# Performance work log

Hardware: AMD Instinct MI355X
Metric: run time of the kernel (lower is better)

Reference implementation:

```python
import jax, jax.numpy as jnp
import numpy as np

K = 15                # top-k codes per token
COMMITMENT_COST = 0.25
N, D, Q = 16384, 256, 8192  # tokens, embed_dim, quant_dim (codebook size)


def setup_inputs() -> dict:
    key = jax.random.key(0)
    k1, k2 = jax.random.split(key)
    z_e = jax.random.normal(k1, (N, D), dtype=jnp.float32)
    # codebook initialized uniform(-1/Q, 1/Q) as in the torch module
    embedding = jax.random.uniform(k2, (Q, D), dtype=jnp.float32,
                                   minval=-1.0 / Q, maxval=1.0 / Q)
    return {"z_e": z_e, "embedding": embedding}


def reference(z_e, embedding):
    # squared L2 distances: [N, Q]
    dist = (jnp.sum(z_e ** 2, axis=1, keepdims=True)
            - 2.0 * (z_e @ embedding.T)
            + jnp.sum(embedding ** 2, axis=1)[None, :])
    # top-k nearest codes (torch.topk(-dist))
    _, top_k_indices = jax.lax.top_k(-dist, K)           # [N, K] int32
    z_q_k = embedding[top_k_indices]                      # [N, K, D] gather
    # k-hot scatter: [N, Q]
    rows = jnp.arange(z_e.shape[0])[:, None]              # [N, 1]
    k_hot = jnp.zeros((z_e.shape[0], embedding.shape[0]), dtype=z_e.dtype)
    k_hot = k_hot.at[rows, top_k_indices].set(1.0)
    z_q = jnp.sum(z_q_k, axis=1)                          # [N, D]
    vq_loss = jnp.mean((z_q - jax.lax.stop_gradient(z_e)) ** 2)
    commitment_loss = jnp.mean((z_e - jax.lax.stop_gradient(z_q)) ** 2)
    total_vq_loss = vq_loss + COMMITMENT_COST * commitment_loss
    # straight-through estimator
    z_q_ste = z_e + jax.lax.stop_gradient(z_q - z_e)
    return (z_q_ste, total_vq_loss, k_hot)
```

## Files before the change

### kernel.cpp

```cpp
#include <hip/hip_runtime.h>


#pragma clang fp contract(off)

#define DIM   256
#define KSEL  15
#define CAP   160
#define NTC   64
#define NTO   32
#define KR    24

typedef short  s16x8 __attribute__((ext_vector_type(8)));
typedef float  f32x4 __attribute__((ext_vector_type(4)));

__device__ inline unsigned short f2bf(float f) {
  unsigned u = __builtin_bit_cast(unsigned, f);
  unsigned r = (u + 0x7FFFu + ((u >> 16) & 1u)) >> 16;
  return (unsigned short)r;
}

__device__ inline void nt_zero4(float* p) {
  f32x4 v = {0.f, 0.f, 0.f, 0.f};
  __builtin_nontemporal_store(v, (f32x4*)p);
}

__global__ __launch_bounds__(256)
void prep(const float* __restrict__ emb, unsigned short* __restrict__ ebf,
          float* __restrict__ Enp, int Q) {
  const int gid = blockIdx.x * 256 + threadIdx.x;
  {
    const int i = gid * 8;
    float4 a = *(const float4*)(emb + i);
    float4 b = *(const float4*)(emb + i + 4);
    ushort4 o0; o0.x = f2bf(a.x); o0.y = f2bf(a.y); o0.z = f2bf(a.z); o0.w = f2bf(a.w);
    ushort4 o1; o1.x = f2bf(b.x); o1.y = f2bf(b.y); o1.z = f2bf(b.z); o1.w = f2bf(b.w);
    *(ushort4*)(ebf + i) = o0;
    *(ushort4*)(ebf + i + 4) = o1;
  }
  if (gid < Q) {
    const float* ep = emb + (size_t)gid * DIM;
    float Eh[2];
    for (int h = 0; h < 2; ++h) {
      const int base = 128 * h;
      float r[8];
#pragma unroll
      for (int q2 = 0; q2 < 8; ++q2) { float v = ep[base + q2]; r[q2] = v * v; }
      for (int i = 8; i < 128; i += 8)
#pragma unroll
        for (int q2 = 0; q2 < 8; ++q2) { float v = ep[base + i + q2]; float sq = v * v; r[q2] = r[q2] + sq; }
      Eh[h] = ((r[0] + r[1]) + (r[2] + r[3])) + ((r[4] + r[5]) + (r[6] + r[7]));
    }
    Enp[gid] = Eh[0] + Eh[1];
  }
}

__global__ __launch_bounds__(512, 2)
void vq_capture(const float* __restrict__ z, const unsigned short* __restrict__ ebf,
                int* __restrict__ cntg, unsigned short* __restrict__ candg,
                int N, int Q) {
  __shared__ union {
    unsigned short zbf[NTC][264];
    struct {
      unsigned short candL[NTC][CAP + 2];
      float          scL[NTC][CAP + 1];
    } c;
  } U;
  __shared__ int   cntL[NTC];
  __shared__ float tauL[NTC];
  __shared__ float red[512];

  const int tid  = threadIdx.x;
  const int lane = tid & 63;
  const int wv   = tid >> 6;
  const int t0   = blockIdx.x * NTC;

  {
    const int rt = tid >> 3, rq = tid & 7;
    const float* zp = z + (size_t)(t0 + rt) * DIM;
    float s = 0.f;
#pragma unroll
    for (int m = 0; m < 8; ++m) {
      float4 v = *(const float4*)(zp + 4 * rq + 32 * m);
      s = __builtin_fmaf(v.x, v.x, s);
      s = __builtin_fmaf(v.y, v.y, s);
      s = __builtin_fmaf(v.z, v.z, s);
      s = __builtin_fmaf(v.w, v.w, s);
      ushort4 o; o.x = f2bf(v.x); o.y = f2bf(v.y); o.z = f2bf(v.z); o.w = f2bf(v.w);
      *(ushort4*)&U.zbf[rt][4 * rq + 32 * m] = o;
    }
    red[tid] = s;
  }
  if (tid < NTC) cntL[tid] = 0;
  __syncthreads();

  if (tid < NTC) {
    float s = 0.f;
    for (int j = 0; j < 8; ++j) s += red[tid * 8 + j];
    const float a = 1.0f / (float)Q;
    tauL[tid] = 2.45f * a * 0.57735027f * sqrtf(s) - 1e-6f;
  }

  s16x8 afrag[4][8];
  {
    const int arow = lane & 15;
    const int kq   = (lane >> 4) * 8;
#pragma unroll
    for (int tt = 0; tt < 4; ++tt) {
#pragma unroll
      for (int ks = 0; ks < 8; ++ks)
        afrag[tt][ks] = *(const s16x8*)&U.zbf[tt * 16 + arow][ks * 32 + kq];
    }
  }
  __syncthreads();

  {
    const int ncw  = Q / 8;
    const int c0w  = wv * ncw;
    const int col  = lane & 15;
    const int kq8  = (lane >> 4) * 8;
    const int rbase = (lane >> 4) * 4;
    const unsigned short* bbase = ebf + ((size_t)(c0w + col) * DIM + kq8);

    uint4 buf0[8], buf1[8];
#pragma unroll
    for (int ks = 0; ks < 8; ++ks) buf0[ks] = *(const uint4*)(bbase + ks * 32);

    for (int it = 0; it < 64; it += 2) {
      {
        const unsigned short* bp = bbase + (size_t)(it + 1) * 16 * DIM;
#pragma unroll
        for (int ks = 0; ks < 8; ++ks) buf1[ks] = *(const uint4*)(bp + ks * 32);
      }
      {
        f32x4 acc0 = {0.f, 0.f, 0.f, 0.f};
        f32x4 acc1 = {0.f, 0.f, 0.f, 0.f};
        f32x4 acc2 = {0.f, 0.f, 0.f, 0.f};
        f32x4 acc3 = {0.f, 0.f, 0.f, 0.f};
#pragma unroll
        for (int ks = 0; ks < 8; ++ks) {
          s16x8 bfv = __builtin_bit_cast(s16x8, buf0[ks]);
          acc0 = __builtin_amdgcn_mfma_f32_16x16x32_bf16(afrag[0][ks], bfv, acc0, 0, 0, 0);
          acc1 = __builtin_amdgcn_mfma_f32_16x16x32_bf16(afrag[1][ks], bfv, acc1, 0, 0, 0);
          acc2 = __builtin_amdgcn_mfma_f32_16x16x32_bf16(afrag[2][ks], bfv, acc2, 0, 0, 0);
          acc3 = __builtin_amdgcn_mfma_f32_16x16x32_bf16(afrag[3][ks], bfv, acc3, 0, 0, 0);
        }
        const int code = c0w + it * 16 + col;
#pragma unroll
        for (int r = 0; r < 4; ++r) {
          const int tk0 = rbase + r;
          if (acc0[r] > tauL[tk0]) {
            int s = atomicAdd(&cntL[tk0], 1);
            if (s < CAP) { U.c.candL[tk0][s] = (unsigned short)code; U.c.scL[tk0][s] = acc0[r]; }
          }
          const int tk1 = 16 + rbase + r;
          if (acc1[r] > tauL[tk1]) {
            int s = atomicAdd(&cntL[tk1], 1);
            if (s < CAP) { U.c.candL[tk1][s] = (unsigned short)code; U.c.scL[tk1][s] = acc1[r]; }
          }
          const int tk2 = 32 + rbase + r;
          if (acc2[r] > tauL[tk2]) {
            int s = atomicAdd(&cntL[tk2], 1);
            if (s < CAP) { U.c.candL[tk2][s] = (unsigned short)code; U.c.scL[tk2][s] = acc2[r]; }
          }
          const int tk3 = 48 + rbase + r;
          if (acc3[r] > tauL[tk3]) {
            int s = atomicAdd(&cntL[tk3], 1);
            if (s < CAP) { U.c.candL[tk3][s] = (unsigned short)code; U.c.scL[tk3][s] = acc3[r]; }
          }
        }
      }
      if (it + 2 < 64) {
        const unsigned short* bp = bbase + (size_t)(it + 2) * 16 * DIM;
#pragma unroll
        for (int ks = 0; ks < 8; ++ks) buf0[ks] = *(const uint4*)(bp + ks * 32);
      }
      {
        f32x4 acc0 = {0.f, 0.f, 0.f, 0.f};
        f32x4 acc1 = {0.f, 0.f, 0.f, 0.f};
        f32x4 acc2 = {0.f, 0.f, 0.f, 0.f};
        f32x4 acc3 = {0.f, 0.f, 0.f, 0.f};
#pragma unroll
        for (int ks = 0; ks < 8; ++ks) {
          s16x8 bfv = __builtin_bit_cast(s16x8, buf1[ks]);
          acc0 = __builtin_amdgcn_mfma_f32_16x16x32_bf16(afrag[0][ks], bfv, acc0, 0, 0, 0);
          acc1 = __builtin_amdgcn_mfma_f32_16x16x32_bf16(afrag[1][ks], bfv, acc1, 0, 0, 0);
          acc2 = __builtin_amdgcn_mfma_f32_16x16x32_bf16(afrag[2][ks], bfv, acc2, 0, 0, 0);
          acc3 = __builtin_amdgcn_mfma_f32_16x16x32_bf16(afrag[3][ks], bfv, acc3, 0, 0, 0);
        }
        const int code = c0w + (it + 1) * 16 + col;
#pragma unroll
        for (int r = 0; r < 4; ++r) {
          const int tk0 = rbase + r;
          if (acc0[r] > tauL[tk0]) {
            int s = atomicAdd(&cntL[tk0], 1);
            if (s < CAP) { U.c.candL[tk0][s] = (unsigned short)code; U.c.scL[tk0][s] = acc0[r]; }
          }
          const int tk1 = 16 + rbase + r;
          if (acc1[r] > tauL[tk1]) {
            int s = atomicAdd(&cntL[tk1], 1);
            if (s < CAP) { U.c.candL[tk1][s] = (unsigned short)code; U.c.scL[tk1][s] = acc1[r]; }
          }
          const int tk2 = 32 + rbase + r;
          if (acc2[r] > tauL[tk2]) {
            int s = atomicAdd(&cntL[tk2], 1);
            if (s < CAP) { U.c.candL[tk2][s] = (unsigned short)code; U.c.scL[tk2][s] = acc2[r]; }
          }
          const int tk3 = 48 + rbase + r;
          if (acc3[r] > tauL[tk3]) {
            int s = atomicAdd(&cntL[tk3], 1);
            if (s < CAP) { U.c.candL[tk3][s] = (unsigned short)code; U.c.scL[tk3][s] = acc3[r]; }
          }
        }
      }
    }
  }
  __syncthreads();

  if ((tid & 7) == 0) {
    const int t = tid >> 3;
    const int m = min(cntL[t], CAP);
    const int keep = min(m, KR);
    for (int k = 0; k < keep; ++k) {
      float bv = -3.4e38f; int bj = 0;
      for (int j = 0; j < m; ++j) {
        float v = U.c.scL[t][j];
        if (v > bv) { bv = v; bj = j; }
      }
      U.c.scL[t][bj] = -3.5e38f;
      candg[(size_t)(t0 + t) * KR + k] = U.c.candL[t][bj];
    }
    cntg[t0 + t] = keep;
  }
}

__global__ __launch_bounds__(256, 2)
void vq_out(const float* __restrict__ z, const float* __restrict__ emb,
            const float* __restrict__ Enp, const int* __restrict__ cntg,
            const unsigned short* __restrict__ candg, float* __restrict__ out,
            int N, int Q) {
  __shared__ __align__(16) float zlds[NTO][DIM + 4];
  __shared__ __align__(16) float ebuf[KR][DIM + 4];
  __shared__ unsigned short cand[NTO][KR];
  __shared__ float sc[NTO][KR + 1];
  __shared__ int   cntL[NTO];
  __shared__ float ArowL[NTO];
  __shared__ int   win[NTO][KSEL];
  __shared__ float red[256];

  const int tid = threadIdx.x;
  const int t0  = blockIdx.x * NTO;
  float* khot = out + (size_t)N * DIM + 1;
  float* pref = khot + (size_t)t0 * Q + 3;
  const int nf4 = (NTO * Q - 4) / 4;

  if (tid < 3) khot[(size_t)t0 * Q + tid] = 0.f;
  if (tid == 3) khot[(size_t)t0 * Q + (size_t)NTO * Q - 1] = 0.f;

  {
    const int rt = tid >> 3, rq = tid & 7;
    const float* zp = z + (size_t)(t0 + rt) * DIM;
    float4 tmp[8];
#pragma unroll
    for (int m = 0; m < 8; ++m) tmp[m] = *(const float4*)(zp + 4 * rq + 32 * m);
#pragma unroll
    for (int m = 0; m < 8; ++m) *(float4*)&zlds[rt][4 * rq + 32 * m] = tmp[m];
  }
  if (tid < NTO) cntL[tid] = min(cntg[t0 + tid], KR);
  __syncthreads();

  for (int i = tid; i < NTO * KR; i += 256) {
    const int t = i / KR, s = i - t * KR;
    cand[t][s] = candg[(size_t)(t0 + t) * KR + s];
  }

  if (tid < NTO) {
    const float* zl = &zlds[tid][0];
    float Ah[2];
    for (int h = 0; h < 2; ++h) {
      const int base = 128 * h;
      float r[8];
#pragma unroll
      for (int q2 = 0; q2 < 8; ++q2) { float v = zl[base + q2]; r[q2] = v * v; }
      for (int i = 8; i < 128; i += 8)
#pragma unroll
        for (int q2 = 0; q2 < 8; ++q2) { float v = zl[base + i + q2]; float sq = v * v; r[q2] = r[q2] + sq; }
      Ah[h] = ((r[0] + r[1]) + (r[2] + r[3])) + ((r[4] + r[5]) + (r[6] + r[7]));
    }
    ArowL[tid] = Ah[0] + Ah[1];
  }
  __syncthreads();

  for (int b = 0; b < NTO; ++b) {
    const int mb = cntL[b];
    {
      const int row = tid >> 3, rq = tid & 7;
      if (row < mb) {
        const float* ep = emb + (size_t)cand[b][row] * DIM;
        float4 tmp[8];
#pragma unroll
        for (int m = 0; m < 8; ++m) tmp[m] = *(const float4*)(ep + 4 * rq + 32 * m);
#pragma unroll
        for (int m = 0; m < 8; ++m) *(float4*)&ebuf[row][4 * rq + 32 * m] = tmp[m];
      }
    }
    {
      const int i0 = b * 2048 + tid;
#pragma unroll
      for (int k = 0; k < 8; ++k) {
        const int i = i0 + k * 256;
        if (i < nf4) nt_zero4(pref + 4 * (size_t)i);
      }
    }
    __syncthreads();
    if ((tid & 7) == 0) {
      const int ci = tid >> 3;
      if (ci < mb) {
        const float* el = &ebuf[ci][0];
        const float* zl = &zlds[b][0];
        float bch = 0.f;
        for (int i = 0; i < 256; i += 8) {
          float4 ea = *(const float4*)(el + i);
          float4 eb = *(const float4*)(el + i + 4);
          float4 za = *(const float4*)(zl + i);
          float4 zb = *(const float4*)(zl + i + 4);
          bch = __builtin_fmaf(za.x, ea.x, bch);
          bch = __builtin_fmaf(za.y, ea.y, bch);
          bch = __builtin_fmaf(za.z, ea.z, bch);
          bch = __builtin_fmaf(za.w, ea.w, bch);
          bch = __builtin_fmaf(zb.x, eb.x, bch);
          bch = __builtin_fmaf(zb.y, eb.y, bch);
          bch = __builtin_fmaf(zb.z, eb.z, bch);
          bch = __builtin_fmaf(zb.w, eb.w, bch);
        }
        const int c = cand[b][ci];
        sc[b][ci] = (ArowL[b] - 2.0f * bch) + Enp[c];
      } else if (ci < KR) {
        sc[b][ci] = 3.4e38f;
      }
    }
    __syncthreads();
  }

  if (tid < NTO) {
    const int m = cntL[tid];
    for (int k = 0; k < KSEL; ++k) {
      float bv = 3.4e38f; int bc = 0x7fffffff; int bj = -1;
      for (int j = 0; j < m; ++j) {
        float v = sc[tid][j]; int c = cand[tid][j];
        if (v < bv || (v == bv && c < bc)) { bv = v; bc = c; bj = j; }
      }
      if (bj >= 0) sc[tid][bj] = 3.5e38f;
      win[tid][k] = (bj >= 0) ? bc : 0;
    }
  }
  __syncthreads();

  {
    const int qt = tid >> 3, qq = tid & 7;
    float4 zq4[8];
#pragma unroll
    for (int m = 0; m < 8; ++m) zq4[m] = make_float4(0.f, 0.f, 0.f, 0.f);
    for (int k = 0; k < KSEL; ++k) {
      const int c = win[qt][k];
      const float* ep = emb + (size_t)c * DIM;
#pragma unroll
      for (int m = 0; m < 8; ++m) {
        float4 e4 = *(const float4*)(ep + 4 * qq + 32 * m);
        zq4[m].x = zq4[m].x + e4.x; zq4[m].y = zq4[m].y + e4.y;
        zq4[m].z = zq4[m].z + e4.z; zq4[m].w = zq4[m].w + e4.w;
      }
    }
    float* op = out + (size_t)(t0 + qt) * DIM;
    float lp = 0.f;
#pragma unroll
    for (int m = 0; m < 8; ++m) {
      float4 zv = *(const float4*)&zlds[qt][4 * qq + 32 * m];
      float4 qv = zq4[m];
      float d0 = qv.x - zv.x, d1 = qv.y - zv.y, d2 = qv.z - zv.z, d3 = qv.w - zv.w;
      float4 o; o.x = zv.x + d0; o.y = zv.y + d1; o.z = zv.z + d2; o.w = zv.w + d3;
      *(float4*)(op + 4 * qq + 32 * m) = o;
      lp = __builtin_fmaf(d0, d0, lp);
      lp = __builtin_fmaf(d1, d1, lp);
      lp = __builtin_fmaf(d2, d2, lp);
      lp = __builtin_fmaf(d3, d3, lp);
    }
    red[tid] = lp;
  }
  __syncthreads();
  for (int s = 128; s > 0; s >>= 1) {
    if (tid < s) red[tid] += red[tid + s];
    __syncthreads();
  }
  if (tid == 0) {
    const float scale = 1.25f / (float)((size_t)N * DIM);
    atomicAdd(out + (size_t)N * DIM, red[0] * scale);
  }

  for (int i = tid; i < NTO * KSEL; i += 256) {
    const int t = i / KSEL, k = i - t * KSEL;
    khot[(size_t)(t0 + t) * Q + win[t][k]] = 1.0f;
  }
}

extern "C" void kernel_launch(void* const* d_in, const int* in_sizes, int n_in,
                              void* d_out, int out_size, void* d_ws, size_t ws_size,
                              hipStream_t stream) {
  const float* z   = (const float*)d_in[0];
  const float* emb = (const float*)d_in[1];
  float* out = (float*)d_out;
  const int N = in_sizes[0] / DIM;
  const int Q = in_sizes[1] / DIM;

  unsigned short* ebf = (unsigned short*)d_ws;
  char* p = (char*)d_ws + (size_t)Q * DIM * 2;
  float* Enp  = (float*)p;           p += (size_t)Q * 4;
  int*   cntg = (int*)p;             p += (size_t)N * 4;
  unsigned short* candg = (unsigned short*)p;

  hipMemsetAsync((char*)d_out + (size_t)N * DIM * sizeof(float), 0, sizeof(float), stream);
  prep<<<dim3((Q * DIM) / (8 * 256)), dim3(256), 0, stream>>>(emb, ebf, Enp, Q);
  vq_capture<<<dim3(N / NTC), dim3(512), 0, stream>>>(z, ebf, cntg, candg, N, Q);
  vq_out<<<dim3(N / NTO), dim3(256), 0, stream>>>(z, emb, Enp, cntg, candg, out, N, Q);
}
```

Measured before the change: 896.0 us.

## Restructure vq_out to one wavefront per token with shuffle-based top-k

Rewrites the final rescoring kernel so that each 64-lane wavefront handles four tokens in turn. Each lane scores one candidate straight from global memory, and the top-15 is picked with a 64-bit key min-reduction over wave shuffles. This replaces block-wide LDS staging of candidate rows, per-token __syncthreads, and single-thread serial selection. The k-hot row zeroing moves to ordinary stores per wave, and the ones are written after a vmcnt wait. In exchange, occupancy rises, but each lane's dot product now reads embedding rows uncoalesced from global memory, and the nontemporal stores for the large zero fill are dropped.

```diff
diff --git a/kernel.cpp b/kernel.cpp
--- a/kernel.cpp
+++ b/kernel.cpp
@@ -7,7 +7,6 @@
 #define KSEL  15
 #define CAP   160
 #define NTC   64
-#define NTO   32
 #define KR    24
 
 typedef short  s16x8 __attribute__((ext_vector_type(8)));
@@ -17,11 +16,6 @@
   unsigned u = __builtin_bit_cast(unsigned, f);
   unsigned r = (u + 0x7FFFu + ((u >> 16) & 1u)) >> 16;
   return (unsigned short)r;
-}
-
-__device__ inline void nt_zero4(float* p) {
-  f32x4 v = {0.f, 0.f, 0.f, 0.f};
-  __builtin_nontemporal_store(v, (f32x4*)p);
 }
 
 __global__ __launch_bounds__(256)
@@ -233,159 +227,133 @@
   }
 }
 
-__global__ __launch_bounds__(256, 2)
+__global__ __launch_bounds__(256, 4)
 void vq_out(const float* __restrict__ z, const float* __restrict__ emb,
             const float* __restrict__ Enp, const int* __restrict__ cntg,
             const unsigned short* __restrict__ candg, float* __restrict__ out,
             int N, int Q) {
-  __shared__ __align__(16) float zlds[NTO][DIM + 4];
-  __shared__ __align__(16) float ebuf[KR][DIM + 4];
-  __shared__ unsigned short cand[NTO][KR];
-  __shared__ float sc[NTO][KR + 1];
-  __shared__ int   cntL[NTO];
-  __shared__ float ArowL[NTO];
-  __shared__ int   win[NTO][KSEL];
+  __shared__ __align__(16) float zld[4][DIM + 4];
   __shared__ float red[256];
 
-  const int tid = threadIdx.x;
-  const int t0  = blockIdx.x * NTO;
+  const int tid  = threadIdx.x;
+  const int lane = tid & 63;
+  const int wv   = tid >> 6;
+  const int gw   = blockIdx.x * 4 + wv;
   float* khot = out + (size_t)N * DIM + 1;
-  float* pref = khot + (size_t)t0 * Q + 3;
-  const int nf4 = (NTO * Q - 4) / 4;
-
-  if (tid < 3) khot[(size_t)t0 * Q + tid] = 0.f;
-  if (tid == 3) khot[(size_t)t0 * Q + (size_t)NTO * Q - 1] = 0.f;
-
-  {
-    const int rt = tid >> 3, rq = tid & 7;
-    const float* zp = z + (size_t)(t0 + rt) * DIM;
-    float4 tmp[8];
-#pragma unroll
-    for (int m = 0; m < 8; ++m) tmp[m] = *(const float4*)(zp + 4 * rq + 32 * m);
-#pragma unroll
-    for (int m = 0; m < 8; ++m) *(float4*)&zlds[rt][4 * rq + 32 * m] = tmp[m];
-  }
-  if (tid < NTO) cntL[tid] = min(cntg[t0 + tid], KR);
-  __syncthreads();
-
-  for (int i = tid; i < NTO * KR; i += 256) {
-    const int t = i / KR, s = i - t * KR;
-    cand[t][s] = candg[(size_t)(t0 + t) * KR + s];
-  }
-
-  if (tid < NTO) {
-    const float* zl = &zlds[tid][0];
-    float Ah[2];
-    for (int h = 0; h < 2; ++h) {
-      const int base = 128 * h;
-      float r[8];
-#pragma unroll
-      for (int q2 = 0; q2 < 8; ++q2) { float v = zl[base + q2]; r[q2] = v * v; }
-      for (int i = 8; i < 128; i += 8)
-#pragma unroll
-        for (int q2 = 0; q2 < 8; ++q2) { float v = zl[base + i + q2]; float sq = v * v; r[q2] = r[q2] + sq; }
-      Ah[h] = ((r[0] + r[1]) + (r[2] + r[3])) + ((r[4] + r[5]) + (r[6] + r[7]));
-    }
-    ArowL[tid] = Ah[0] + Ah[1];
-  }
-  __syncthreads();
-
-  for (int b = 0; b < NTO; ++b) {
-    const int mb = cntL[b];
-    {
-      const int row = tid >> 3, rq = tid & 7;
-      if (row < mb) {
-        const float* ep = emb + (size_t)cand[b][row] * DIM;
-        float4 tmp[8];
-#pragma unroll
-        for (int m = 0; m < 8; ++m) tmp[m] = *(const float4*)(ep + 4 * rq + 32 * m);
-#pragma unroll
-        for (int m = 0; m < 8; ++m) *(float4*)&ebuf[row][4 * rq + 32 * m] = tmp[m];
-      }
-    }
-    {
-      const int i0 = b * 2048 + tid;
-#pragma unroll
-      for (int k = 0; k < 8; ++k) {
-        const int i = i0 + k * 256;
-        if (i < nf4) nt_zero4(pref + 4 * (size_t)i);
-      }
-    }
-    __syncthreads();
-    if ((tid & 7) == 0) {
-      const int ci = tid >> 3;
-      if (ci < mb) {
-        const float* el = &ebuf[ci][0];
-        const float* zl = &zlds[b][0];
-        float bch = 0.f;
-        for (int i = 0; i < 256; i += 8) {
-          float4 ea = *(const float4*)(el + i);
-          float4 eb = *(const float4*)(el + i + 4);
-          float4 za = *(const float4*)(zl + i);
-          float4 zb = *(const float4*)(zl + i + 4);
-          bch = __builtin_fmaf(za.x, ea.x, bch);
-          bch = __builtin_fmaf(za.y, ea.y, bch);
-          bch = __builtin_fmaf(za.z, ea.z, bch);
-          bch = __builtin_fmaf(za.w, ea.w, bch);
-          bch = __builtin_fmaf(zb.x, eb.x, bch);
-          bch = __builtin_fmaf(zb.y, eb.y, bch);
-          bch = __builtin_fmaf(zb.z, eb.z, bch);
-          bch = __builtin_fmaf(zb.w, eb.w, bch);
-        }
-        const int c = cand[b][ci];
-        sc[b][ci] = (ArowL[b] - 2.0f * bch) + Enp[c];
-      } else if (ci < KR) {
-        sc[b][ci] = 3.4e38f;
-      }
-    }
-    __syncthreads();
-  }
-
-  if (tid < NTO) {
-    const int m = cntL[tid];
-    for (int k = 0; k < KSEL; ++k) {
-      float bv = 3.4e38f; int bc = 0x7fffffff; int bj = -1;
-      for (int j = 0; j < m; ++j) {
-        float v = sc[tid][j]; int c = cand[tid][j];
-        if (v < bv || (v == bv && c < bc)) { bv = v; bc = c; bj = j; }
-      }
-      if (bj >= 0) sc[tid][bj] = 3.5e38f;
-      win[tid][k] = (bj >= 0) ? bc : 0;
-    }
-  }
-  __syncthreads();
-
-  {
-    const int qt = tid >> 3, qq = tid & 7;
-    float4 zq4[8];
-#pragma unroll
-    for (int m = 0; m < 8; ++m) zq4[m] = make_float4(0.f, 0.f, 0.f, 0.f);
-    for (int k = 0; k < KSEL; ++k) {
-      const int c = win[qt][k];
-      const float* ep = emb + (size_t)c * DIM;
-#pragma unroll
-      for (int m = 0; m < 8; ++m) {
-        float4 e4 = *(const float4*)(ep + 4 * qq + 32 * m);
-        zq4[m].x = zq4[m].x + e4.x; zq4[m].y = zq4[m].y + e4.y;
-        zq4[m].z = zq4[m].z + e4.z; zq4[m].w = zq4[m].w + e4.w;
-      }
-    }
-    float* op = out + (size_t)(t0 + qt) * DIM;
-    float lp = 0.f;
-#pragma unroll
-    for (int m = 0; m < 8; ++m) {
-      float4 zv = *(const float4*)&zlds[qt][4 * qq + 32 * m];
-      float4 qv = zq4[m];
-      float d0 = qv.x - zv.x, d1 = qv.y - zv.y, d2 = qv.z - zv.z, d3 = qv.w - zv.w;
+
+  float lpacc = 0.f;
+
+  for (int ti = 0; ti < 4; ++ti) {
+    const int t = gw * 4 + ti;
+
+    {
+      const float4 v = *(const float4*)(z + (size_t)t * DIM + 4 * lane);
+      *(float4*)&zld[wv][4 * lane] = v;
+    }
+    const int mb = min(cntg[t], KR);
+    const int c_mine = (lane < mb) ? (int)candg[(size_t)t * KR + lane] : 0;
+
+    __builtin_amdgcn_s_waitcnt(0);
+
+    float Arow;
+    {
+      float Aval = 0.f;
+      if (lane == 0) {
+        const float* zl = &zld[wv][0];
+        float Ah[2];
+        for (int h = 0; h < 2; ++h) {
+          const int base = 128 * h;
+          float r[8];
+#pragma unroll
+          for (int q2 = 0; q2 < 8; ++q2) { float v = zl[base + q2]; r[q2] = v * v; }
+          for (int i = 8; i < 128; i += 8)
+#pragma unroll
+            for (int q2 = 0; q2 < 8; ++q2) { float v = zl[base + i + q2]; float sq = v * v; r[q2] = r[q2] + sq; }
+          Ah[h] = ((r[0] + r[1]) + (r[2] + r[3])) + ((r[4] + r[5]) + (r[6] + r[7]));
+        }
+        Aval = Ah[0] + Ah[1];
+      }
+      Arow = __shfl(Aval, 0);
+    }
+
+    float scv = 3.4e38f;
+    if (lane < mb) {
+      const float* el = emb + (size_t)c_mine * DIM;
+      const float* zl = &zld[wv][0];
+      float bch = 0.f;
+      for (int i = 0; i < 256; i += 8) {
+        float4 ea = *(const float4*)(el + i);
+        float4 eb = *(const float4*)(el + i + 4);
+        float4 za = *(const float4*)(zl + i);
+        float4 zb = *(const float4*)(zl + i + 4);
+        bch = __builtin_fmaf(za.x, ea.x, bch);
+        bch = __builtin_fmaf(za.y, ea.y, bch);
+        bch = __builtin_fmaf(za.z, ea.z, bch);
+        bch = __builtin_fmaf(za.w, ea.w, bch);
+        bch = __builtin_fmaf(zb.x, eb.x, bch);
+        bch = __builtin_fmaf(zb.y, eb.y, bch);
+        bch = __builtin_fmaf(zb.z, eb.z, bch);
+        bch = __builtin_fmaf(zb.w, eb.w, bch);
+      }
+      scv = (Arow - 2.0f * bch) + Enp[c_mine];
+    }
+
+    int mywin = 0;
+    {
+      unsigned okey = __builtin_bit_cast(unsigned, scv);
+      okey = (okey & 0x80000000u) ? ~okey : (okey | 0x80000000u);
+      unsigned long long key = (lane < mb)
+          ? (((unsigned long long)okey << 32) | (unsigned)c_mine)
+          : 0xFFFFFFFFFFFFFFFFull;
+      for (int k = 0; k < KSEL; ++k) {
+        unsigned long long m = key;
+#pragma unroll
+        for (int d = 1; d < 64; d <<= 1) {
+          unsigned long long o = __shfl_xor(m, d);
+          m = (o < m) ? o : m;
+        }
+        int wcode = ((unsigned)(m >> 32) == 0xFFFFFFFFu) ? 0 : (int)(unsigned)(m & 0xFFFFFFFFull);
+        if (lane == k) mywin = wcode;
+        if (key == m) key = 0xFFFFFFFFFFFFFFFFull;
+      }
+    }
+
+    {
+      float* rowp = khot + (size_t)t * Q;
+      if (lane < 3) rowp[lane] = 0.f;
+      if (lane == 3) rowp[Q - 1] = 0.f;
+      float4* p4 = (float4*)(rowp + 3);
+      const f32x4 zv = {0.f, 0.f, 0.f, 0.f};
+#pragma unroll
+      for (int i = 0; i < 32; ++i) {
+        const int idx = lane + 64 * i;
+        if (idx < 2047) *(f32x4*)&p4[idx] = zv;
+      }
+    }
+    asm volatile("s_waitcnt vmcnt(0)" ::: "memory");
+    if (lane < KSEL) khot[(size_t)t * Q + mywin] = 1.0f;
+
+    {
+      float4 zq4 = make_float4(0.f, 0.f, 0.f, 0.f);
+      for (int k = 0; k < KSEL; ++k) {
+        const int c = __shfl(mywin, k);
+        const float4 e4 = *(const float4*)(emb + (size_t)c * DIM + 4 * lane);
+        zq4.x = zq4.x + e4.x; zq4.y = zq4.y + e4.y;
+        zq4.z = zq4.z + e4.z; zq4.w = zq4.w + e4.w;
+      }
+      const float4 zv = *(const float4*)&zld[wv][4 * lane];
+      float d0 = zq4.x - zv.x, d1 = zq4.y - zv.y, d2 = zq4.z - zv.z, d3 = zq4.w - zv.w;
       float4 o; o.x = zv.x + d0; o.y = zv.y + d1; o.z = zv.z + d2; o.w = zv.w + d3;
-      *(float4*)(op + 4 * qq + 32 * m) = o;
-      lp = __builtin_fmaf(d0, d0, lp);
-      lp = __builtin_fmaf(d1, d1, lp);
-      lp = __builtin_fmaf(d2, d2, lp);
-      lp = __builtin_fmaf(d3, d3, lp);
-    }
-    red[tid] = lp;
-  }
+      *(float4*)(out + (size_t)t * DIM + 4 * lane) = o;
+      lpacc = __builtin_fmaf(d0, d0, lpacc);
+      lpacc = __builtin_fmaf(d1, d1, lpacc);
+      lpacc = __builtin_fmaf(d2, d2, lpacc);
+      lpacc = __builtin_fmaf(d3, d3, lpacc);
+    }
+    __builtin_amdgcn_s_waitcnt(0);
+  }
+
+  red[tid] = lpacc;
   __syncthreads();
   for (int s = 128; s > 0; s >>= 1) {
     if (tid < s) red[tid] += red[tid + s];
@@ -394,11 +362,6 @@
   if (tid == 0) {
     const float scale = 1.25f / (float)((size_t)N * DIM);
     atomicAdd(out + (size_t)N * DIM, red[0] * scale);
-  }
-
-  for (int i = tid; i < NTO * KSEL; i += 256) {
-    const int t = i / KSEL, k = i - t * KSEL;
-    khot[(size_t)(t0 + t) * Q + win[t][k]] = 1.0f;
   }
 }
 
@@ -420,5 +383,5 @@
   hipMemsetAsync((char*)d_out + (size_t)N * DIM * sizeof(float), 0, sizeof(float), stream);
   prep<<<dim3((Q * DIM) / (8 * 256)), dim3(256), 0, stream>>>(emb, ebf, Enp, Q);
   vq_capture<<<dim3(N / NTC), dim3(512), 0, stream>>>(z, ebf, cntg, candg, N, Q);
-  vq_out<<<dim3(N / NTO), dim3(256), 0, stream>>>(z, emb, Enp, cntg, candg, out, N, Q);
-}
+  vq_out<<<dim3(N / (4 * 4)), dim3(256), 0, stream>>>(z, emb, Enp, cntg, candg, out, N, Q);
+}
```

Result: no change. 901.8 us (+0.6%).
